# Kernel optimization log

Measured on AMD Instinct MI355X. Metric: run time of the kernel, lower is better.

The kernel has to match this reference:

```python
import jax, jax.numpy as jnp
import numpy as np

S, DIM, H, HD = 8192, 1280, 16, 80
B, L = 8, 1024  # 8 equal-length packed segments


def setup_inputs() -> dict:
    key = jax.random.key(0)
    ks = jax.random.split(key, 6)
    hidden_states = jax.random.normal(ks[0], (S, DIM), dtype=jnp.float32)
    Wqkv = jax.random.normal(ks[1], (DIM, 3 * DIM), dtype=jnp.float32) * (DIM ** -0.5)
    bqkv = jax.random.normal(ks[2], (3 * DIM,), dtype=jnp.float32) * 0.02
    Wproj = jax.random.normal(ks[3], (DIM, DIM), dtype=jnp.float32) * (DIM ** -0.5)
    bproj = jax.random.normal(ks[4], (DIM,), dtype=jnp.float32) * 0.02
    # rotary tables: per-token position within its segment, repeated-half layout
    pos = jnp.tile(jnp.arange(L, dtype=jnp.float32), B)  # [S]
    inv_freq = 1.0 / (10000.0 ** (jnp.arange(0, HD, 2, dtype=jnp.float32) / HD))  # [HD/2]
    ang = pos[:, None] * inv_freq[None, :]  # [S, HD/2]
    ang = jnp.concatenate([ang, ang], axis=-1)  # [S, HD]
    cos, sin = jnp.cos(ang), jnp.sin(ang)
    cu_seqlens = (jnp.arange(B + 1, dtype=jnp.int32) * L)
    return {"hidden_states": hidden_states, "cos": cos, "sin": sin,
            "Wqkv": Wqkv, "bqkv": bqkv, "Wproj": Wproj, "bproj": bproj,
            "cu_seqlens": cu_seqlens, "max_seqlen": L}


def _rotate_half(x):
    x1, x2 = jnp.split(x, 2, axis=-1)
    return jnp.concatenate([-x2, x1], axis=-1)


def reference(hidden_states, cos, sin, Wqkv, bqkv, Wproj, bproj, cu_seqlens, max_seqlen):
    s = hidden_states.shape[0]
    nseg = cu_seqlens.shape[0] - 1
    scale = HD ** -0.5
    qkv = (hidden_states @ Wqkv + bqkv).reshape(s, 3, H, HD)
    q, k, v = qkv[:, 0], qkv[:, 1], qkv[:, 2]  # each [S, H, HD]
    c = cos[:, None, :]
    sn = sin[:, None, :]
    q = q * c + _rotate_half(q) * sn
    k = k * c + _rotate_half(k) * sn
    # equal-length packed segments: [S,H,HD] -> [B,L,H,HD]
    q = q.reshape(nseg, max_seqlen, H, HD)
    k = k.reshape(nseg, max_seqlen, H, HD)
    v = v.reshape(nseg, max_seqlen, H, HD)
    scores = jnp.einsum("blhd,bmhd->bhlm", q, k) * scale
    probs = jax.nn.softmax(scores, axis=-1)
    out = jnp.einsum("bhlm,bmhd->blhd", probs, v).reshape(s, DIM)
    return out @ Wproj + bproj
```

## Files before the change

### kernel.cpp

```cpp
#include <hip/hip_runtime.h>
#include <hip/hip_bf16.h>
#include <stdint.h>

typedef __bf16 bf16_t;
typedef __bf16 bf16x8 __attribute__((ext_vector_type(8)));
typedef float f32x4 __attribute__((ext_vector_type(4)));
typedef float f32x16 __attribute__((ext_vector_type(16)));

#define S_TOK 8192
#define DIM   1280
#define NH    16
#define HD    80
#define LSEQ  1024
#define N_QKV 3840

__device__ __forceinline__ void gload16(const bf16_t* g, void* l) {
  __builtin_amdgcn_global_load_lds(
      (__attribute__((address_space(1))) uint32_t*)g,
      (__attribute__((address_space(3))) uint32_t*)l, 16, 0, 0);
}

__global__ __launch_bounds__(256) void k_conv_bf16(const float* __restrict__ in,
                                                   bf16_t* __restrict__ out) {
  int g = blockIdx.x * 256 + threadIdx.x;
  const float4* p = reinterpret_cast<const float4*>(in) + (size_t)g * 2;
  float4 v0 = p[0], v1 = p[1];
  bf16x8 o;
  o[0] = (bf16_t)v0.x; o[1] = (bf16_t)v0.y; o[2] = (bf16_t)v0.z; o[3] = (bf16_t)v0.w;
  o[4] = (bf16_t)v1.x; o[5] = (bf16_t)v1.y; o[6] = (bf16_t)v1.z; o[7] = (bf16_t)v1.w;
  *reinterpret_cast<bf16x8*>(out + (size_t)g * 8) = o;
}

__global__ __launch_bounds__(256) void k_transpose_bf16(const float* __restrict__ W,
                                                        bf16_t* __restrict__ Wt,
                                                        int K, int N) {
  __shared__ float tile[32][33];
  int n0 = blockIdx.x * 32, k0 = blockIdx.y * 32;
  int tx = threadIdx.x, ty = threadIdx.y;
#pragma unroll
  for (int j = 0; j < 32; j += 8)
    tile[ty + j][tx] = W[(size_t)(k0 + ty + j) * N + n0 + tx];
  __syncthreads();
#pragma unroll
  for (int j = 0; j < 32; j += 8)
    Wt[(size_t)(n0 + ty + j) * K + k0 + tx] = (bf16_t)tile[tx][ty + j];
}

template <bool OUT_BF16>
__global__ __launch_bounds__(512, 2) void k_gemm8(const bf16_t* __restrict__ A,
                                                  const bf16_t* __restrict__ Bt,
                                                  const float* __restrict__ bias,
                                                  void* __restrict__ Cout,
                                                  int N) {
  constexpr int K = 1280;
  constexpr int NT = K / 64;
  __shared__ __align__(16) char smem[131072];
  const int nb = N >> 8;
  const int cpx = (int)gridDim.x >> 3;
  const int wg = ((int)blockIdx.x & 7) * cpx + ((int)blockIdx.x >> 3);
  const int bm = wg / nb, bn = wg % nb;
  const int tid = threadIdx.x, lane = tid & 63, w = tid >> 6;
  const int wm = w >> 2, wn = w & 3;
  const int l15 = lane & 15, lg = lane >> 4;

  const bf16_t* Ab = A + (size_t)(bm * 256) * K;
  const bf16_t* Bb = Bt + (size_t)(bn * 256) * K;

  const int srow = w * 8 + (lane >> 3);
  const int scol = ((lane & 7) ^ (lane >> 3)) * 8;

  float bv4[4];
#pragma unroll
  for (int nf = 0; nf < 4; ++nf)
    bv4[nf] = bias[bn * 256 + wn * 64 + nf * 16 + l15];
  asm volatile("" :: "v"(bv4[0]), "v"(bv4[1]), "v"(bv4[2]), "v"(bv4[3]) : "memory");
  asm volatile("s_waitcnt vmcnt(0)" ::: "memory");

  char* const sm = smem;
  auto stageA = [&](int buf, int g, int k0) {
    gload16(Ab + (size_t)(g * 64 + srow) * K + k0 + scol,
            sm + buf * 65536 + g * 8192 + w * 1024);
  };
  auto stageB = [&](int buf, int g, int k0) {
    gload16(Bb + (size_t)(g * 64 + srow) * K + k0 + scol,
            sm + buf * 65536 + 32768 + g * 8192 + w * 1024);
  };

  f32x4 acc[8][4];
#pragma unroll
  for (int i = 0; i < 8; ++i)
#pragma unroll
    for (int j = 0; j < 4; ++j) acc[i][j] = (f32x4){0.f, 0.f, 0.f, 0.f};

#pragma unroll
  for (int g = 0; g < 4; ++g) { stageA(0, g, 0); stageB(0, g, 0); }

#pragma unroll 1
  for (int T = 0; T < NT; ++T) {
    const int buf = T & 1, nbuf = buf ^ 1;
    const int k1 = (T + 1) * 64;
    if (T + 1 < NT) {
      stageA(nbuf, 0, k1);
      stageA(nbuf, 1, k1);
      asm volatile("s_waitcnt vmcnt(2)\n\ts_barrier" ::: "memory");
      stageA(nbuf, 2, k1); stageA(nbuf, 3, k1);
      stageB(nbuf, 0, k1); stageB(nbuf, 1, k1);
      stageB(nbuf, 2, k1); stageB(nbuf, 3, k1);
    } else {
      asm volatile("s_waitcnt vmcnt(0)\n\ts_barrier" ::: "memory");
    }
    const char* Abase = sm + buf * 65536;
    const char* Bbase = Abase + 32768;
#pragma unroll
    for (int kk = 0; kk < 2; ++kk) {
      const int cb = kk * 64 + lg * 16;
      bf16x8 bfv[4];
#pragma unroll
      for (int nf = 0; nf < 4; ++nf) {
        const int row = wn * 64 + nf * 16 + l15;
        bfv[nf] = *reinterpret_cast<const bf16x8*>(Bbase + row * 128 + (cb ^ ((row & 7) << 4)));
      }
#pragma unroll
      for (int mg = 0; mg < 2; ++mg) {
        bf16x8 af[4];
#pragma unroll
        for (int mf = 0; mf < 4; ++mf) {
          const int row = wm * 128 + mg * 64 + mf * 16 + l15;
          af[mf] = *reinterpret_cast<const bf16x8*>(Abase + row * 128 + (cb ^ ((row & 7) << 4)));
        }
        __builtin_amdgcn_s_setprio(1);
#pragma unroll
        for (int mf = 0; mf < 4; ++mf)
#pragma unroll
          for (int nf = 0; nf < 4; ++nf)
            acc[mg * 4 + mf][nf] =
                __builtin_amdgcn_mfma_f32_16x16x32_bf16(af[mf], bfv[nf], acc[mg * 4 + mf][nf], 0, 0, 0);
        __builtin_amdgcn_s_setprio(0);
      }
    }
  }

  const int rg = lg << 2;
#pragma unroll
  for (int nf = 0; nf < 4; ++nf) {
    const int col = bn * 256 + wn * 64 + nf * 16 + l15;
    const float bv = bv4[nf];
#pragma unroll
    for (int m8 = 0; m8 < 8; ++m8) {
      const int row0 = bm * 256 + wm * 128 + m8 * 16 + rg;
#pragma unroll
      for (int r = 0; r < 4; ++r) {
        float v = acc[m8][nf][r] + bv;
        if (OUT_BF16)
          reinterpret_cast<bf16_t*>(Cout)[(size_t)(row0 + r) * N + col] = (bf16_t)v;
        else
          reinterpret_cast<float*>(Cout)[(size_t)(row0 + r) * N + col] = v;
      }
    }
  }
}

__global__ __launch_bounds__(256) void k_rope(bf16_t* __restrict__ qkv,
                                              const float* __restrict__ cosT,
                                              const float* __restrict__ sinT) {
  const float QS = 0.11180339887498949f * 1.4426950408889634f;
  int g = blockIdx.x * 256 + threadIdx.x;
  int c = g % 5;
  int h = (g / 5) & 15;
  int s = g / 80;
  const int d0 = c * 8;
  float cs[8], sn[8];
#pragma unroll
  for (int j = 0; j < 8; ++j) {
    cs[j] = cosT[s * 80 + d0 + j];
    sn[j] = sinT[s * 80 + d0 + j];
  }
  size_t base = (size_t)s * N_QKV + h * 80 + d0;
#pragma unroll
  for (int part = 0; part < 2; ++part) {
    const float sc = (part == 0) ? QS : 1.0f;
    bf16_t* p0 = qkv + base + part * 1280;
    bf16_t* p1 = p0 + 40;
    bf16x8 a = *reinterpret_cast<bf16x8*>(p0);
    bf16x8 b = *reinterpret_cast<bf16x8*>(p1);
    bf16x8 oa, ob;
#pragma unroll
    for (int j = 0; j < 8; ++j) {
      float x = (float)a[j], y = (float)b[j];
      oa[j] = (bf16_t)((x * cs[j] - y * sn[j]) * sc);
      ob[j] = (bf16_t)((y * cs[j] + x * sn[j]) * sc);
    }
    *reinterpret_cast<bf16x8*>(p0) = oa;
    *reinterpret_cast<bf16x8*>(p1) = ob;
  }
}

__global__ __launch_bounds__(256) void k_vtrans(const bf16_t* __restrict__ qkv,
                                                bf16_t* __restrict__ vtg) {
  __shared__ bf16_t T[64][88];
  int sh = blockIdx.x >> 4;
  int kt = blockIdx.x & 15;
  int seg = sh >> 4, h = sh & 15;
  int kv0 = kt * 64;
  int tid = threadIdx.x;
#pragma unroll
  for (int i = 0; i < 3; ++i) {
    int c = tid + i * 256;
    if (c < 640) {
      int r = c / 10, ch = c - r * 10;
      *reinterpret_cast<uint4*>(&T[r][ch * 8]) =
        *reinterpret_cast<const uint4*>(qkv + (size_t)(seg * 1024 + kv0 + r) * N_QKV + 2 * DIM + h * 80 + ch * 8);
    }
  }
  __syncthreads();
#pragma unroll
  for (int i = 0; i < 3; ++i) {
    int c = tid + i * 256;
    if (c < 640) {
      int d = c >> 3, co = c & 7;
      bf16x8 o;
#pragma unroll
      for (int j = 0; j < 8; ++j) {
        int kp = co * 8 + j;
        int kv = (kp & ~12) | (((kp >> 2) & 1) << 3) | (((kp >> 3) & 1) << 2);
        o[j] = T[kv][d];
      }
      *reinterpret_cast<bf16x8*>(vtg + ((size_t)(sh * 80 + d)) * 1024 + kv0 + co * 8) = o;
    }
  }
}

__global__ __launch_bounds__(512, 2) void k_attn2(const bf16_t* __restrict__ qkv,
                                                  const bf16_t* __restrict__ vtg,
                                                  bf16_t* __restrict__ outp) {
  __shared__ __align__(16) char smem[47104];
  bf16_t* KsB = (bf16_t*)smem;
  bf16_t* VsB = (bf16_t*)(smem + 22528);

  const int bid = blockIdx.x;
  const int seg = bid & 7, qt = (bid >> 3) & 3, h = bid >> 5;
  const int tid = threadIdx.x, lane = tid & 63, w = tid >> 6;
  const int l31 = lane & 31, hi = lane >> 5;
  const int q0 = seg * 1024 + qt * 256;

  const bf16_t* kbase = qkv + ((size_t)seg * 1024) * N_QKV + DIM + h * 80;
  const bf16_t* vbase = vtg + ((size_t)(seg * 16 + h) * 80) * 1024;

  bf16x8 qf[5];
  {
    const bf16_t* qp = qkv + (size_t)(q0 + w * 32 + l31) * N_QKV + h * 80 + hi * 8;
#pragma unroll
    for (int ks = 0; ks < 5; ++ks) qf[ks] = *reinterpret_cast<const bf16x8*>(qp + ks * 16);
  }

  const uint4 ones4 = {0x3F803F80u, 0x3F803F80u, 0x3F803F80u, 0x3F803F80u};
  uint4 kreg[2], vreg[2];
  auto issue = [&](int kv0) {
#pragma unroll
    for (int i = 0; i < 2; ++i) {
      int c = tid + i * 512;
      if (c < 640) {
        int r = c / 10, ch = c - r * 10;
        kreg[i] = *reinterpret_cast<const uint4*>(kbase + (size_t)(kv0 + r) * N_QKV + ch * 8);
      }
    }
#pragma unroll
    for (int i = 0; i < 2; ++i) {
      int c = tid + i * 512;
      if (c < 768) {
        int d = c >> 3, ch = c & 7;
        uint4 v = {0u, 0u, 0u, 0u};
        if (d < 80) v = *reinterpret_cast<const uint4*>(vbase + (size_t)d * 1024 + kv0 + ch * 8);
        else if (d == 80) v = ones4;
        vreg[i] = v;
      }
    }
  };
  auto commit = [&](int b) {
    bf16_t* Kb = KsB + b * 5632;
    bf16_t* Vb = VsB + b * 6144;
#pragma unroll
    for (int i = 0; i < 2; ++i) {
      int c = tid + i * 512;
      if (c < 640) {
        int r = c / 10, ch = c - r * 10;
        *reinterpret_cast<uint4*>(Kb + r * 88 + ch * 8) = kreg[i];
      }
    }
#pragma unroll
    for (int i = 0; i < 2; ++i) {
      int c = tid + i * 512;
      if (c < 768) {
        int d = c >> 3, ch = c & 7;
        *reinterpret_cast<uint4*>(Vb + d * 64 + ((ch ^ (d & 7)) << 3)) = vreg[i];
      }
    }
  };

  f32x16 o0, o1, o2;
#pragma unroll
  for (int r = 0; r < 16; ++r) { o0[r] = 0.f; o1[r] = 0.f; o2[r] = 0.f; }
  float mrun = -1e30f;

  issue(0);
  commit(0);
  __syncthreads();
  int cur = 0;

  for (int t = 0; t < 16; ++t) {
    if (t < 15) issue((t + 1) * 64);
    const bf16_t* Kb = KsB + cur * 5632;
    const bf16_t* Vb = VsB + cur * 6144;

    f32x16 st0, st1;
#pragma unroll
    for (int r = 0; r < 16; ++r) { st0[r] = 0.f; st1[r] = 0.f; }
    __builtin_amdgcn_s_setprio(1);
#pragma unroll
    for (int ks = 0; ks < 5; ++ks) {
      bf16x8 k0 = *reinterpret_cast<const bf16x8*>(Kb + l31 * 88 + ks * 16 + hi * 8);
      bf16x8 k1 = *reinterpret_cast<const bf16x8*>(Kb + (32 + l31) * 88 + ks * 16 + hi * 8);
      st0 = __builtin_amdgcn_mfma_f32_32x32x16_bf16(k0, qf[ks], st0, 0, 0, 0);
      st1 = __builtin_amdgcn_mfma_f32_32x32x16_bf16(k1, qf[ks], st1, 0, 0, 0);
    }
    __builtin_amdgcn_s_setprio(0);

    float mt[16];
#pragma unroll
    for (int r = 0; r < 16; ++r) mt[r] = fmaxf(st0[r], st1[r]);
#pragma unroll
    for (int s2 = 8; s2 >= 1; s2 >>= 1)
#pragma unroll
      for (int r = 0; r < s2; ++r) mt[r] = fmaxf(mt[r], mt[r + s2]);
    float mx = fmaxf(mt[0], __shfl_xor(mt[0], 32));
    if (!__all(mx <= mrun + 6.0f)) {
      float mnew = fmaxf(mrun, mx);
      float corr = __builtin_exp2f(mrun - mnew);
      mrun = mnew;
#pragma unroll
      for (int r = 0; r < 16; ++r) { o0[r] *= corr; o1[r] *= corr; o2[r] *= corr; }
    }
#pragma unroll
    for (int r = 0; r < 16; ++r) st0[r] = __builtin_exp2f(st0[r] - mrun);
#pragma unroll
    for (int r = 0; r < 16; ++r) st1[r] = __builtin_exp2f(st1[r] - mrun);

    bf16x8 pb[4];
#pragma unroll
    for (int u = 0; u < 2; ++u)
#pragma unroll
      for (int j = 0; j < 8; ++j) {
        pb[u][j]     = (bf16_t)st0[u * 8 + j];
        pb[2 + u][j] = (bf16_t)st1[u * 8 + j];
      }

    __builtin_amdgcn_s_setprio(1);
#pragma unroll
    for (int ks2 = 0; ks2 < 4; ++ks2) {
      {
        int row = l31;
        bf16x8 vf = *reinterpret_cast<const bf16x8*>(Vb + row * 64 + ((((ks2 << 1) + hi) ^ (row & 7)) << 3));
        o0 = __builtin_amdgcn_mfma_f32_32x32x16_bf16(vf, pb[ks2], o0, 0, 0, 0);
      }
      {
        int row = 32 + l31;
        bf16x8 vf = *reinterpret_cast<const bf16x8*>(Vb + row * 64 + ((((ks2 << 1) + hi) ^ (row & 7)) << 3));
        o1 = __builtin_amdgcn_mfma_f32_32x32x16_bf16(vf, pb[ks2], o1, 0, 0, 0);
      }
      {
        int row = 64 + l31;
        bf16x8 vf = *reinterpret_cast<const bf16x8*>(Vb + row * 64 + ((((ks2 << 1) + hi) ^ (row & 7)) << 3));
        o2 = __builtin_amdgcn_mfma_f32_32x32x16_bf16(vf, pb[ks2], o2, 0, 0, 0);
      }
    }
    __builtin_amdgcn_s_setprio(0);

    if (t < 15) commit(cur ^ 1);
    __syncthreads();
    cur ^= 1;
  }

  float sp = o2[8] + __shfl_xor(o2[8], 32);
  float inv = 1.0f / sp;

  bf16_t* Osm = (bf16_t*)smem;
  const int qrow = w * 32 + l31;
#pragma unroll
  for (int r = 0; r < 16; ++r) {
    int crow = (r & 3) + 8 * (r >> 2) + 4 * hi;
    Osm[qrow * 88 + crow]      = (bf16_t)(o0[r] * inv);
    Osm[qrow * 88 + 32 + crow] = (bf16_t)(o1[r] * inv);
    if (r < 8) Osm[qrow * 88 + 64 + crow] = (bf16_t)(o2[r] * inv);
  }
  __syncthreads();
#pragma unroll
  for (int i = 0; i < 5; ++i) {
    int c = tid + i * 512;
    int q = c / 10, ch = c - q * 10;
    uint4 v = *reinterpret_cast<const uint4*>(Osm + q * 88 + ch * 8);
    *reinterpret_cast<uint4*>(outp + (size_t)(q0 + q) * DIM + h * 80 + ch * 8) = v;
  }
}

extern "C" void kernel_launch(void* const* d_in, const int* in_sizes, int n_in,
                              void* d_out, int out_size, void* d_ws, size_t ws_size,
                              hipStream_t stream) {
  const float* hs    = (const float*)d_in[0];
  const float* cosT  = (const float*)d_in[1];
  const float* sinT  = (const float*)d_in[2];
  const float* Wqkv  = (const float*)d_in[3];
  const float* bqkv  = (const float*)d_in[4];
  const float* Wproj = (const float*)d_in[5];
  const float* bproj = (const float*)d_in[6];
  (void)in_sizes; (void)n_in; (void)out_size; (void)ws_size;

  char* ws = (char*)d_ws;
  bf16_t* hsb  = (bf16_t*)(ws);
  bf16_t* w1t  = (bf16_t*)(ws + 20971520);
  bf16_t* w2t  = (bf16_t*)(ws + 30801920);
  bf16_t* qkvb = (bf16_t*)(ws + 34078720);
  bf16_t* attn = (bf16_t*)(ws + 96993280);
  bf16_t* vtg  = hsb;

  k_conv_bf16<<<5120, 256, 0, stream>>>(hs, hsb);
  k_transpose_bf16<<<dim3(120, 40), dim3(32, 8), 0, stream>>>(Wqkv, w1t, 1280, 3840);
  k_transpose_bf16<<<dim3(40, 40), dim3(32, 8), 0, stream>>>(Wproj, w2t, 1280, 1280);
  k_gemm8<true><<<480, 512, 0, stream>>>(hsb, w1t, bqkv, (void*)qkvb, 3840);
  k_rope<<<2560, 256, 0, stream>>>(qkvb, cosT, sinT);
  k_vtrans<<<2048, 256, 0, stream>>>(qkvb, vtg);
  k_attn2<<<512, 512, 0, stream>>>(qkvb, vtg, attn);
  k_gemm8<false><<<160, 512, 0, stream>>>(attn, w2t, bproj, d_out, 1280);
}
```

Measured before the change: 254.1 us.

## Read K/V fragments directly from global memory in attention, dropping LDS staging

The attention kernel no longer stages K and V tiles through double-buffered shared memory with per-tile barriers. Each lane now loads its MFMA operand fragments straight from global memory (L2/cache), and a small padded buffer supplies the ones/zero rows used for the row-sum trick. Shared memory drops to just the output staging buffer, and the occupancy hint is raised to 4 blocks. The trade-off is redundant global/L2 traffic from every wave reading the same K/V, and load latency that is no longer hidden by explicit prefetch.

After: 322.9 us. 27.1% more time.

```diff
diff --git a/kernel.cpp b/kernel.cpp
--- a/kernel.cpp
+++ b/kernel.cpp
@@ -230,21 +230,25 @@
   }
 }
 
-__global__ __launch_bounds__(512, 2) void k_attn2(const bf16_t* __restrict__ qkv,
+__global__ __launch_bounds__(256) void k_padinit(bf16_t* __restrict__ vpad) {
+  int g = blockIdx.x * 256 + threadIdx.x;
+  const uint4 ones4 = {0x3F803F80u, 0x3F803F80u, 0x3F803F80u, 0x3F803F80u};
+  const uint4 z4 = {0u, 0u, 0u, 0u};
+  reinterpret_cast<uint4*>(vpad)[g] = (g < 128) ? ones4 : z4;
+}
+
+__global__ __launch_bounds__(512, 4) void k_attn2(const bf16_t* __restrict__ qkv,
                                                   const bf16_t* __restrict__ vtg,
+                                                  const bf16_t* __restrict__ vpad,
                                                   bf16_t* __restrict__ outp) {
-  __shared__ __align__(16) char smem[47104];
-  bf16_t* KsB = (bf16_t*)smem;
-  bf16_t* VsB = (bf16_t*)(smem + 22528);
+  __shared__ __align__(16) bf16_t Osm[256 * 88];
 
   const int bid = blockIdx.x;
   const int seg = bid & 7, qt = (bid >> 3) & 3, h = bid >> 5;
   const int tid = threadIdx.x, lane = tid & 63, w = tid >> 6;
   const int l31 = lane & 31, hi = lane >> 5;
   const int q0 = seg * 1024 + qt * 256;
-
-  const bf16_t* kbase = qkv + ((size_t)seg * 1024) * N_QKV + DIM + h * 80;
-  const bf16_t* vbase = vtg + ((size_t)(seg * 16 + h) * 80) * 1024;
+  const int sh = seg * 16 + h;
 
   bf16x8 qf[5];
   {
@@ -253,75 +257,31 @@
     for (int ks = 0; ks < 5; ++ks) qf[ks] = *reinterpret_cast<const bf16x8*>(qp + ks * 16);
   }
 
-  const uint4 ones4 = {0x3F803F80u, 0x3F803F80u, 0x3F803F80u, 0x3F803F80u};
-  uint4 kreg[2], vreg[2];
-  auto issue = [&](int kv0) {
-#pragma unroll
-    for (int i = 0; i < 2; ++i) {
-      int c = tid + i * 512;
-      if (c < 640) {
-        int r = c / 10, ch = c - r * 10;
-        kreg[i] = *reinterpret_cast<const uint4*>(kbase + (size_t)(kv0 + r) * N_QKV + ch * 8);
-      }
-    }
-#pragma unroll
-    for (int i = 0; i < 2; ++i) {
-      int c = tid + i * 512;
-      if (c < 768) {
-        int d = c >> 3, ch = c & 7;
-        uint4 v = {0u, 0u, 0u, 0u};
-        if (d < 80) v = *reinterpret_cast<const uint4*>(vbase + (size_t)d * 1024 + kv0 + ch * 8);
-        else if (d == 80) v = ones4;
-        vreg[i] = v;
-      }
-    }
-  };
-  auto commit = [&](int b) {
-    bf16_t* Kb = KsB + b * 5632;
-    bf16_t* Vb = VsB + b * 6144;
-#pragma unroll
-    for (int i = 0; i < 2; ++i) {
-      int c = tid + i * 512;
-      if (c < 640) {
-        int r = c / 10, ch = c - r * 10;
-        *reinterpret_cast<uint4*>(Kb + r * 88 + ch * 8) = kreg[i];
-      }
-    }
-#pragma unroll
-    for (int i = 0; i < 2; ++i) {
-      int c = tid + i * 512;
-      if (c < 768) {
-        int d = c >> 3, ch = c & 7;
-        *reinterpret_cast<uint4*>(Vb + d * 64 + ((ch ^ (d & 7)) << 3)) = vreg[i];
-      }
-    }
-  };
+  const bf16_t* k0p = qkv + (size_t)(seg * 1024 + l31) * N_QKV + DIM + h * 80 + hi * 8;
+  const bf16_t* k1p = k0p + (size_t)32 * N_QKV;
+  const bf16_t* v0p = vtg + (size_t)(sh * 80 + l31) * 1024;
+  const bf16_t* v1p = vtg + (size_t)(sh * 80 + 32 + l31) * 1024;
+  const int r2 = 64 + l31;
+  const bf16_t* v2p = (r2 < 80) ? (vtg + (size_t)(sh * 80 + r2) * 1024)
+                                : (vpad + (size_t)(r2 - 80) * 1024);
 
   f32x16 o0, o1, o2;
 #pragma unroll
   for (int r = 0; r < 16; ++r) { o0[r] = 0.f; o1[r] = 0.f; o2[r] = 0.f; }
   float mrun = -1e30f;
 
-  issue(0);
-  commit(0);
-  __syncthreads();
-  int cur = 0;
-
+#pragma unroll 1
   for (int t = 0; t < 16; ++t) {
-    if (t < 15) issue((t + 1) * 64);
-    const bf16_t* Kb = KsB + cur * 5632;
-    const bf16_t* Vb = VsB + cur * 6144;
-
     f32x16 st0, st1;
 #pragma unroll
     for (int r = 0; r < 16; ++r) { st0[r] = 0.f; st1[r] = 0.f; }
     __builtin_amdgcn_s_setprio(1);
 #pragma unroll
     for (int ks = 0; ks < 5; ++ks) {
-      bf16x8 k0 = *reinterpret_cast<const bf16x8*>(Kb + l31 * 88 + ks * 16 + hi * 8);
-      bf16x8 k1 = *reinterpret_cast<const bf16x8*>(Kb + (32 + l31) * 88 + ks * 16 + hi * 8);
-      st0 = __builtin_amdgcn_mfma_f32_32x32x16_bf16(k0, qf[ks], st0, 0, 0, 0);
-      st1 = __builtin_amdgcn_mfma_f32_32x32x16_bf16(k1, qf[ks], st1, 0, 0, 0);
+      bf16x8 a0 = *reinterpret_cast<const bf16x8*>(k0p + ks * 16);
+      bf16x8 a1 = *reinterpret_cast<const bf16x8*>(k1p + ks * 16);
+      st0 = __builtin_amdgcn_mfma_f32_32x32x16_bf16(a0, qf[ks], st0, 0, 0, 0);
+      st1 = __builtin_amdgcn_mfma_f32_32x32x16_bf16(a1, qf[ks], st1, 0, 0, 0);
     }
     __builtin_amdgcn_s_setprio(0);
 
@@ -357,33 +317,24 @@
     __builtin_amdgcn_s_setprio(1);
 #pragma unroll
     for (int ks2 = 0; ks2 < 4; ++ks2) {
-      {
-        int row = l31;
-        bf16x8 vf = *reinterpret_cast<const bf16x8*>(Vb + row * 64 + ((((ks2 << 1) + hi) ^ (row & 7)) << 3));
-        o0 = __builtin_amdgcn_mfma_f32_32x32x16_bf16(vf, pb[ks2], o0, 0, 0, 0);
-      }
-      {
-        int row = 32 + l31;
-        bf16x8 vf = *reinterpret_cast<const bf16x8*>(Vb + row * 64 + ((((ks2 << 1) + hi) ^ (row & 7)) << 3));
-        o1 = __builtin_amdgcn_mfma_f32_32x32x16_bf16(vf, pb[ks2], o1, 0, 0, 0);
-      }
-      {
-        int row = 64 + l31;
-        bf16x8 vf = *reinterpret_cast<const bf16x8*>(Vb + row * 64 + ((((ks2 << 1) + hi) ^ (row & 7)) << 3));
-        o2 = __builtin_amdgcn_mfma_f32_32x32x16_bf16(vf, pb[ks2], o2, 0, 0, 0);
-      }
+      const int off = ((ks2 << 1) | hi) << 3;
+      bf16x8 b0 = *reinterpret_cast<const bf16x8*>(v0p + off);
+      bf16x8 b1 = *reinterpret_cast<const bf16x8*>(v1p + off);
+      bf16x8 b2 = *reinterpret_cast<const bf16x8*>(v2p + off);
+      o0 = __builtin_amdgcn_mfma_f32_32x32x16_bf16(b0, pb[ks2], o0, 0, 0, 0);
+      o1 = __builtin_amdgcn_mfma_f32_32x32x16_bf16(b1, pb[ks2], o1, 0, 0, 0);
+      o2 = __builtin_amdgcn_mfma_f32_32x32x16_bf16(b2, pb[ks2], o2, 0, 0, 0);
     }
     __builtin_amdgcn_s_setprio(0);
 
-    if (t < 15) commit(cur ^ 1);
-    __syncthreads();
-    cur ^= 1;
+    k0p += (size_t)64 * N_QKV;
+    k1p += (size_t)64 * N_QKV;
+    v0p += 64; v1p += 64; v2p += 64;
   }
 
   float sp = o2[8] + __shfl_xor(o2[8], 32);
   float inv = 1.0f / sp;
 
-  bf16_t* Osm = (bf16_t*)smem;
   const int qrow = w * 32 + l31;
 #pragma unroll
   for (int r = 0; r < 16; ++r) {
@@ -421,6 +372,7 @@
   bf16_t* qkvb = (bf16_t*)(ws + 34078720);
   bf16_t* attn = (bf16_t*)(ws + 96993280);
   bf16_t* vtg  = hsb;
+  bf16_t* vpad = w1t;
 
   k_conv_bf16<<<5120, 256, 0, stream>>>(hs, hsb);
   k_transpose_bf16<<<dim3(120, 40), dim3(32, 8), 0, stream>>>(Wqkv, w1t, 1280, 3840);
@@ -428,6 +380,7 @@
   k_gemm8<true><<<480, 512, 0, stream>>>(hsb, w1t, bqkv, (void*)qkvb, 3840);
   k_rope<<<2560, 256, 0, stream>>>(qkvb, cosT, sinT);
   k_vtrans<<<2048, 256, 0, stream>>>(qkvb, vtg);
-  k_attn2<<<512, 512, 0, stream>>>(qkvb, vtg, attn);
+  k_padinit<<<8, 256, 0, stream>>>(vpad);
+  k_attn2<<<512, 512, 0, stream>>>(qkvb, vtg, vpad, attn);
   k_gemm8<false><<<160, 512, 0, stream>>>(attn, w2t, bproj, d_out, 1280);
 }
```

## Software-pipeline attention: overlap QK of next tile with PV of previous

Applied to the files above, without the earlier changes.

Restructures the attention main loop so each iteration computes QK^T for tile t while doing the PV MFMAs for tile t-1, with a prologue and epilogue around the loop. V gets a triple-buffered LDS ring and K keeps a double buffer, now with a 128-element XOR-swizzled row layout in place of 88-element padding. The aim is to hide the softmax and exp latency behind independent matrix-core work and to cut LDS bank conflicts on K reads. In exchange, LDS use per block grows to about 68 KB, which puts pressure on the two-blocks-per-CU occupancy target, and register pressure rises because the st and pb values stay live across stages.

Measured after the change: 250.0 us. No clear change (-1.6%).

```diff
diff --git a/kernel.cpp b/kernel.cpp
--- a/kernel.cpp
+++ b/kernel.cpp
@@ -233,14 +233,15 @@
 __global__ __launch_bounds__(512, 2) void k_attn2(const bf16_t* __restrict__ qkv,
                                                   const bf16_t* __restrict__ vtg,
                                                   bf16_t* __restrict__ outp) {
-  __shared__ __align__(16) char smem[47104];
+  __shared__ __align__(16) char smem[69632];
   bf16_t* KsB = (bf16_t*)smem;
-  bf16_t* VsB = (bf16_t*)(smem + 22528);
+  bf16_t* VsB = (bf16_t*)(smem + 32768);
 
   const int bid = blockIdx.x;
   const int seg = bid & 7, qt = (bid >> 3) & 3, h = bid >> 5;
   const int tid = threadIdx.x, lane = tid & 63, w = tid >> 6;
   const int l31 = lane & 31, hi = lane >> 5;
+  const int sw = l31 & 7;
   const int q0 = seg * 1024 + qt * 256;
 
   const bf16_t* kbase = qkv + ((size_t)seg * 1024) * N_QKV + DIM + h * 80;
@@ -276,15 +277,15 @@
       }
     }
   };
-  auto commit = [&](int b) {
-    bf16_t* Kb = KsB + b * 5632;
-    bf16_t* Vb = VsB + b * 6144;
+  auto commit = [&](int kb, int vb) {
+    bf16_t* Kb = KsB + kb * 8192;
+    bf16_t* Vb = VsB + vb * 6144;
 #pragma unroll
     for (int i = 0; i < 2; ++i) {
       int c = tid + i * 512;
       if (c < 640) {
         int r = c / 10, ch = c - r * 10;
-        *reinterpret_cast<uint4*>(Kb + r * 88 + ch * 8) = kreg[i];
+        *reinterpret_cast<uint4*>(Kb + r * 128 + ((ch ^ (r & 7)) << 3)) = kreg[i];
       }
     }
 #pragma unroll
@@ -301,30 +302,40 @@
 #pragma unroll
   for (int r = 0; r < 16; ++r) { o0[r] = 0.f; o1[r] = 0.f; o2[r] = 0.f; }
   float mrun = -1e30f;
-
-  issue(0);
-  commit(0);
-  __syncthreads();
-  int cur = 0;
-
-  for (int t = 0; t < 16; ++t) {
-    if (t < 15) issue((t + 1) * 64);
-    const bf16_t* Kb = KsB + cur * 5632;
-    const bf16_t* Vb = VsB + cur * 6144;
-
-    f32x16 st0, st1;
+  f32x16 st0, st1;
+  bf16x8 pb[4];
+
+  auto qk = [&](int kb) {
 #pragma unroll
     for (int r = 0; r < 16; ++r) { st0[r] = 0.f; st1[r] = 0.f; }
+    const bf16_t* Kb = KsB + kb * 8192;
     __builtin_amdgcn_s_setprio(1);
 #pragma unroll
     for (int ks = 0; ks < 5; ++ks) {
-      bf16x8 k0 = *reinterpret_cast<const bf16x8*>(Kb + l31 * 88 + ks * 16 + hi * 8);
-      bf16x8 k1 = *reinterpret_cast<const bf16x8*>(Kb + (32 + l31) * 88 + ks * 16 + hi * 8);
+      const int so = (((ks << 1) | hi) ^ sw) << 3;
+      bf16x8 k0 = *reinterpret_cast<const bf16x8*>(Kb + l31 * 128 + so);
+      bf16x8 k1 = *reinterpret_cast<const bf16x8*>(Kb + (32 + l31) * 128 + so);
       st0 = __builtin_amdgcn_mfma_f32_32x32x16_bf16(k0, qf[ks], st0, 0, 0, 0);
       st1 = __builtin_amdgcn_mfma_f32_32x32x16_bf16(k1, qf[ks], st1, 0, 0, 0);
     }
     __builtin_amdgcn_s_setprio(0);
-
+  };
+  auto pv = [&](int vb) {
+    const bf16_t* Vb = VsB + vb * 6144;
+    __builtin_amdgcn_s_setprio(1);
+#pragma unroll
+    for (int ks2 = 0; ks2 < 4; ++ks2) {
+      const int so = (((ks2 << 1) | hi) ^ sw) << 3;
+      bf16x8 v0 = *reinterpret_cast<const bf16x8*>(Vb + l31 * 64 + so);
+      bf16x8 v1 = *reinterpret_cast<const bf16x8*>(Vb + (32 + l31) * 64 + so);
+      bf16x8 v2 = *reinterpret_cast<const bf16x8*>(Vb + (64 + l31) * 64 + so);
+      o0 = __builtin_amdgcn_mfma_f32_32x32x16_bf16(v0, pb[ks2], o0, 0, 0, 0);
+      o1 = __builtin_amdgcn_mfma_f32_32x32x16_bf16(v1, pb[ks2], o1, 0, 0, 0);
+      o2 = __builtin_amdgcn_mfma_f32_32x32x16_bf16(v2, pb[ks2], o2, 0, 0, 0);
+    }
+    __builtin_amdgcn_s_setprio(0);
+  };
+  auto softmax_pack = [&]() {
     float mt[16];
 #pragma unroll
     for (int r = 0; r < 16; ++r) mt[r] = fmaxf(st0[r], st1[r]);
@@ -344,8 +355,6 @@
     for (int r = 0; r < 16; ++r) st0[r] = __builtin_exp2f(st0[r] - mrun);
 #pragma unroll
     for (int r = 0; r < 16; ++r) st1[r] = __builtin_exp2f(st1[r] - mrun);
-
-    bf16x8 pb[4];
 #pragma unroll
     for (int u = 0; u < 2; ++u)
 #pragma unroll
@@ -353,32 +362,28 @@
         pb[u][j]     = (bf16_t)st0[u * 8 + j];
         pb[2 + u][j] = (bf16_t)st1[u * 8 + j];
       }
-
-    __builtin_amdgcn_s_setprio(1);
-#pragma unroll
-    for (int ks2 = 0; ks2 < 4; ++ks2) {
-      {
-        int row = l31;
-        bf16x8 vf = *reinterpret_cast<const bf16x8*>(Vb + row * 64 + ((((ks2 << 1) + hi) ^ (row & 7)) << 3));
-        o0 = __builtin_amdgcn_mfma_f32_32x32x16_bf16(vf, pb[ks2], o0, 0, 0, 0);
-      }
-      {
-        int row = 32 + l31;
-        bf16x8 vf = *reinterpret_cast<const bf16x8*>(Vb + row * 64 + ((((ks2 << 1) + hi) ^ (row & 7)) << 3));
-        o1 = __builtin_amdgcn_mfma_f32_32x32x16_bf16(vf, pb[ks2], o1, 0, 0, 0);
-      }
-      {
-        int row = 64 + l31;
-        bf16x8 vf = *reinterpret_cast<const bf16x8*>(Vb + row * 64 + ((((ks2 << 1) + hi) ^ (row & 7)) << 3));
-        o2 = __builtin_amdgcn_mfma_f32_32x32x16_bf16(vf, pb[ks2], o2, 0, 0, 0);
-      }
-    }
-    __builtin_amdgcn_s_setprio(0);
-
-    if (t < 15) commit(cur ^ 1);
+  };
+
+  issue(0);
+  commit(0, 0);
+  __syncthreads();
+  issue(64);
+  qk(0);
+  softmax_pack();
+  commit(1, 1);
+  __syncthreads();
+
+#pragma unroll 1
+  for (int t = 1; t < 16; ++t) {
+    if (t < 15) issue((t + 1) * 64);
+    qk(t & 1);
+    pv((t - 1) % 3);
+    softmax_pack();
+    if (t < 15) commit((t + 1) & 1, (t + 1) % 3);
     __syncthreads();
-    cur ^= 1;
-  }
+  }
+  pv(0);
+  __syncthreads();
 
   float sp = o2[8] + __shfl_xor(o2[8], 32);
   float inv = 1.0f / sp;
```
